# Optimization experiments

Measured on AMD Instinct MI355X. Metric: run time of the kernel, lower is better.

Reference implementation:

```python
import jax, jax.numpy as jnp
import numpy as np

B, S, T, V, E, H = 32, 64, 64, 32000, 512, 1024


def setup_inputs() -> dict:
    key = jax.random.key(0)
    ks = jax.random.split(key, 12)
    n = lambda k, shp, s=0.05: jax.random.normal(k, shp, dtype=jnp.float32) * s
    return {
        "src": jax.random.randint(ks[0], (B, S), 0, V, dtype=jnp.int32),
        "tgt": jax.random.randint(ks[1], (B, T), 0, V, dtype=jnp.int32),
        "enc_emb": n(ks[2], (V, E)),
        "dec_emb": n(ks[3], (V, E)),
        "Wih_e": n(ks[4], (E, H)), "bih_e": jnp.zeros((H,), jnp.float32),
        "Whh_e": n(ks[5], (H, H)), "bhh_e": jnp.zeros((H,), jnp.float32),
        "Wih_d": n(ks[6], (E, H)), "bih_d": jnp.zeros((H,), jnp.float32),
        "Whh_d": n(ks[7], (H, H)), "bhh_d": jnp.zeros((H,), jnp.float32),
        "Wout": n(ks[8], (H, V)), "bout": jnp.zeros((V,), jnp.float32),
    }


def reference(src, tgt, enc_emb, dec_emb, Wih_e, bih_e, Whh_e, bhh_e,
              Wih_d, bih_d, Whh_d, bhh_d, Wout, bout):
    # Embedding lookups: [B, S, E] / [B, T, E]
    src_e = enc_emb[src]
    tgt_e = dec_emb[tgt]
    # Precompute input-to-hidden projections for every timestep (same math,
    # batched into one GEMM each): [B, S, H] / [B, T, H]
    x_e = jnp.einsum('bse,eh->bsh', src_e, Wih_e) + bih_e
    x_d = jnp.einsum('bte,eh->bth', tgt_e, Wih_d) + bih_d

    h0 = jnp.zeros((src.shape[0], Whh_e.shape[0]), dtype=x_e.dtype)

    def enc_step(h, x):  # h,x: [B, H]
        h = jnp.tanh(x + h @ Whh_e + bhh_e)
        return h, None

    h_enc, _ = jax.lax.scan(enc_step, h0, jnp.swapaxes(x_e, 0, 1))

    def dec_step(h, x):
        h = jnp.tanh(x + h @ Whh_d + bhh_d)
        return h, h

    _, hs = jax.lax.scan(dec_step, h_enc, jnp.swapaxes(x_d, 0, 1))  # [T, B, H]

    logits = jnp.einsum('tbh,hv->tbv', hs, Wout) + bout  # [T, B, V]
    out = jax.nn.log_softmax(logits, axis=-1)
    return jnp.swapaxes(out, 0, 1)  # [B, T, V]
```

## Files before the change

kernel.cpp:

```cpp
#include <hip/hip_runtime.h>
#include <hip/hip_bf16.h>
#include <math.h>

#define B_ 32
#define S_ 64
#define T_ 64
#define V_ 32000
#define E_ 512
#define H_ 1024

typedef __attribute__((ext_vector_type(8))) short short8;
typedef __attribute__((ext_vector_type(4))) float f32x4;

static __device__ __forceinline__ unsigned short f2bf(float f) {
  union { float f; unsigned u; } c; c.f = f;
  unsigned r = (c.u + 0x7fffu + ((c.u >> 16) & 1u)) >> 16;
  return (unsigned short)r;
}

__global__ __launch_bounds__(128)
void gather_f32(const int* __restrict__ idx, const float* __restrict__ emb,
                float* __restrict__ dst) {
  int r = blockIdx.x;
  int tid = threadIdx.x;
  int tok = idx[r];
  float4 v = *(const float4*)(emb + (size_t)tok * E_ + tid * 4);
  *(float4*)(dst + (size_t)r * E_ + tid * 4) = v;
}

__global__ __launch_bounds__(256)
void dgemm_bias(const float* __restrict__ A, const float* __restrict__ B,
                const float* __restrict__ bias, float* __restrict__ C,
                int M, int N, int K) {
  __shared__ float As[32][65];
  __shared__ float Bs[32][64];
  const int nbm = M >> 6;
  const int bm = blockIdx.x % nbm;
  const int bn = blockIdx.x / nbm;
  const int tid = threadIdx.x;
  const int tr = tid >> 4, tc = tid & 15;
  double acc[4][4] = {};

  for (int kt = 0; kt < K; kt += 32) {
    {
      int arow = tid >> 3, acol = (tid & 7) * 4;
#pragma unroll
      for (int p = 0; p < 2; ++p) {
        int r = arow + p * 32;
        float4 v = *(const float4*)(A + (size_t)(bm * 64 + r) * K + kt + acol);
        As[acol + 0][r] = v.x; As[acol + 1][r] = v.y;
        As[acol + 2][r] = v.z; As[acol + 3][r] = v.w;
      }
      int brow = tid >> 4, bcol = (tid & 15) * 4;
#pragma unroll
      for (int p = 0; p < 2; ++p) {
        int r = brow + p * 16;
        float4 v = *(const float4*)(B + (size_t)(kt + r) * N + bn * 64 + bcol);
        *(float4*)(&Bs[r][bcol]) = v;
      }
    }
    __syncthreads();
#pragma unroll
    for (int k = 0; k < 32; ++k) {
      double a[4], b[4];
#pragma unroll
      for (int i = 0; i < 4; ++i) a[i] = (double)As[k][tr * 4 + i];
#pragma unroll
      for (int j = 0; j < 4; ++j) b[j] = (double)Bs[k][tc * 4 + j];
#pragma unroll
      for (int i = 0; i < 4; ++i)
#pragma unroll
        for (int j = 0; j < 4; ++j) acc[i][j] = fma(a[i], b[j], acc[i][j]);
    }
    __syncthreads();
  }
#pragma unroll
  for (int i = 0; i < 4; ++i) {
    int gm = bm * 64 + tr * 4 + i;
    int gn = bn * 64 + tc * 4;
    float4 o;
    o.x = (float)(acc[i][0] + (double)bias[gn + 0]);
    o.y = (float)(acc[i][1] + (double)bias[gn + 1]);
    o.z = (float)(acc[i][2] + (double)bias[gn + 2]);
    o.w = (float)(acc[i][3] + (double)bias[gn + 3]);
    *(float4*)(C + (size_t)gm * N + gn) = o;
  }
}

__global__ __launch_bounds__(256)
void transpose_f32(const float* __restrict__ W, float* __restrict__ WT,
                   int K, int N) {
  __shared__ float t[64][65];
  int k0 = blockIdx.x * 64;
  int n0 = blockIdx.y * 64;
  int tid = threadIdx.x;
  int r = tid >> 4, c4 = tid & 15;
#pragma unroll
  for (int i = 0; i < 4; ++i) {
    int row = r + i * 16;
    float4 v = *(const float4*)(W + (size_t)(k0 + row) * N + n0 + c4 * 4);
    t[row][c4 * 4 + 0] = v.x; t[row][c4 * 4 + 1] = v.y;
    t[row][c4 * 4 + 2] = v.z; t[row][c4 * 4 + 3] = v.w;
  }
  __syncthreads();
#pragma unroll
  for (int i = 0; i < 4; ++i) {
    int n = r + i * 16;
    float4 o;
    o.x = t[c4 * 4 + 0][n]; o.y = t[c4 * 4 + 1][n];
    o.z = t[c4 * 4 + 2][n]; o.w = t[c4 * 4 + 3][n];
    *(float4*)(WT + (size_t)(n0 + n) * K + k0 + c4 * 4) = o;
  }
}

__global__ __launch_bounds__(256)
void transpose_bf16(const float* __restrict__ W, unsigned short* __restrict__ WT,
                    int K, int N) {
  __shared__ float t[64][65];
  int k0 = blockIdx.x * 64;
  int n0 = blockIdx.y * 64;
  int tid = threadIdx.x;
  int r = tid >> 4, c4 = tid & 15;
#pragma unroll
  for (int i = 0; i < 4; ++i) {
    int row = r + i * 16;
    float4 v = *(const float4*)(W + (size_t)(k0 + row) * N + n0 + c4 * 4);
    t[row][c4 * 4 + 0] = v.x; t[row][c4 * 4 + 1] = v.y;
    t[row][c4 * 4 + 2] = v.z; t[row][c4 * 4 + 3] = v.w;
  }
  __syncthreads();
#pragma unroll
  for (int i = 0; i < 4; ++i) {
    int n = r + i * 16;
    ushort4 o;
    o.x = f2bf(t[c4 * 4 + 0][n]); o.y = f2bf(t[c4 * 4 + 1][n]);
    o.z = f2bf(t[c4 * 4 + 2][n]); o.w = f2bf(t[c4 * 4 + 3][n]);
    *(ushort4*)(WT + (size_t)(n0 + n) * K + k0 + c4 * 4) = o;
  }
}

__global__ __launch_bounds__(256)
void gemm_bt_swap(const unsigned short* __restrict__ A, const unsigned short* __restrict__ BT,
                  const float* __restrict__ bias, float* __restrict__ C,
                  int M, int N, int K) {
  __shared__ unsigned short As[128 * 64];
  __shared__ unsigned short Bs[128 * 64];
  const int nbm = M >> 7;
  int idx = blockIdx.x;
  const int cpx = gridDim.x >> 3;
  idx = (idx & 7) * cpx + (idx >> 3);
  const int bm = idx % nbm;
  const int bn = idx / nbm;
  const int tid = threadIdx.x;
  const int lane = tid & 63;
  const int wr = (tid >> 6) >> 1;
  const int wc = (tid >> 6) & 1;

  f32x4 acc[4][4] = {};

  for (int kt = 0; kt < K; kt += 64) {
#pragma unroll
    for (int i = 0; i < 4; ++i) {
      int c = i * 256 + tid;
      int row = c >> 3, col8 = c & 7;
      int sw = col8 ^ (row & 7);
      short8 av = *(const short8*)(A + (size_t)(bm * 128 + row) * K + kt + col8 * 8);
      short8 bv = *(const short8*)(BT + (size_t)(bn * 128 + row) * K + kt + col8 * 8);
      *(short8*)(As + row * 64 + sw * 8) = av;
      *(short8*)(Bs + row * 64 + sw * 8) = bv;
    }
    __syncthreads();
#pragma unroll
    for (int kk = 0; kk < 64; kk += 32) {
      int kc = (kk + ((lane >> 4) << 3)) >> 3;
      short8 af[4], bfr[4];
#pragma unroll
      for (int mi = 0; mi < 4; ++mi) {
        int row = wr * 64 + mi * 16 + (lane & 15);
        af[mi] = *(const short8*)(As + row * 64 + ((kc ^ (row & 7)) << 3));
      }
#pragma unroll
      for (int ni = 0; ni < 4; ++ni) {
        int row = wc * 64 + ni * 16 + (lane & 15);
        bfr[ni] = *(const short8*)(Bs + row * 64 + ((kc ^ (row & 7)) << 3));
      }
#pragma unroll
      for (int mi = 0; mi < 4; ++mi)
#pragma unroll
        for (int ni = 0; ni < 4; ++ni)
          acc[mi][ni] = __builtin_amdgcn_mfma_f32_16x16x32_bf16(
              af[mi], bfr[ni], acc[mi][ni], 0, 0, 0);
    }
    __syncthreads();
  }

  const int cq = (lane >> 4) << 2;
  const int cn = lane & 15;
#pragma unroll
  for (int mi = 0; mi < 4; ++mi) {
#pragma unroll
    for (int ni = 0; ni < 4; ++ni) {
      int gn = bn * 128 + wc * 64 + ni * 16 + cn;
      float bv = bias[gn];
#pragma unroll
      for (int q = 0; q < 4; ++q) {
        int gm = bm * 128 + wr * 64 + mi * 16 + cq + q;
        int b = gm & (B_ - 1);
        int t = gm >> 5;
        __builtin_nontemporal_store(acc[mi][ni][q] + bv,
                                    &C[((size_t)b * T_ + t) * N + gn]);
      }
    }
  }
}

__global__ __launch_bounds__(512)
void rnn_scan_grp2(const float* __restrict__ xe, const float* __restrict__ xd,
                   const float* __restrict__ WTe, const float* __restrict__ WTd,
                   const float* __restrict__ bhhE, const float* __restrict__ bhhD,
                   float* __restrict__ hA, float* __restrict__ hB,
                   unsigned short* __restrict__ hsb, unsigned* __restrict__ bar) {
  __shared__ float hl[4 * 1024];
  const int tid = threadIdx.x;
  const int grp = blockIdx.x & 7;
  const int jslot = blockIdx.x >> 3;
  const int jbase = jslot * 32;
  const int bg = grp * 4;
  const int w = tid >> 6;
  const int l = tid & 63;
  unsigned* mybar = bar + grp * 32;

  const int a = 8 * (l & 1) + 4 * ((l >> 1) & 1) + 2 * ((l >> 2) & 1) +
                ((l >> 3) & 1);
  const int lb = a >> 2;
  const int gb = bg + lb;
  const int gj = jbase + w * 4 + (a & 3);
  const float bje = bhhE[gj];
  const float bjd = bhhD[gj];

  float4 wreg[4][4];
  {
    const float* wsrc = WTe + (size_t)(jbase + w * 4) * 1024;
#pragma unroll
    for (int i = 0; i < 4; ++i) {
      int g = l + 64 * i;
#pragma unroll
      for (int ji = 0; ji < 4; ++ji)
        wreg[i][ji] = *(const float4*)(wsrc + (size_t)ji * 1024 + g * 4);
    }
  }

  for (int t = 0; t < 128; ++t) {
    if (t == 64) {
      const float* wsrc = WTd + (size_t)(jbase + w * 4) * 1024;
#pragma unroll
      for (int i = 0; i < 4; ++i) {
        int g = l + 64 * i;
#pragma unroll
        for (int ji = 0; ji < 4; ++ji)
          wreg[i][ji] = *(const float4*)(wsrc + (size_t)ji * 1024 + g * 4);
      }
    }
    const bool enc = (t < 64);
    const int s = t & 63;
    const float* __restrict__ h_in = (t & 1) ? hB : hA;
    float* __restrict__ h_out = (t & 1) ? hA : hB;
    const float* __restrict__ x = enc ? xe : xd;

    float xv = x[((size_t)gb * 64 + s) * H_ + gj];

    {
      const float* hsrc = h_in + bg * H_;
      float v[8];
#pragma unroll
      for (int u = 0; u < 8; ++u)
        v[u] = __hip_atomic_load(hsrc + u * 512 + tid, __ATOMIC_RELAXED,
                                 __HIP_MEMORY_SCOPE_AGENT);
#pragma unroll
      for (int u = 0; u < 8; ++u)
        hl[u * 512 + tid] = v[u];
    }
    __syncthreads();

    double acc[4][4];
#pragma unroll
    for (int bi = 0; bi < 4; ++bi)
#pragma unroll
      for (int ji = 0; ji < 4; ++ji) acc[bi][ji] = 0.;

#pragma unroll
    for (int i = 0; i < 4; ++i) {
      int g = l + 64 * i;
      float4 hv[4];
#pragma unroll
      for (int bi = 0; bi < 4; ++bi)
        hv[bi] = *(const float4*)(hl + bi * 1024 + g * 4);
#pragma unroll
      for (int bi = 0; bi < 4; ++bi)
#pragma unroll
        for (int ji = 0; ji < 4; ++ji) {
          acc[bi][ji] = fma((double)hv[bi].x, (double)wreg[i][ji].x, acc[bi][ji]);
          acc[bi][ji] = fma((double)hv[bi].y, (double)wreg[i][ji].y, acc[bi][ji]);
          acc[bi][ji] = fma((double)hv[bi].z, (double)wreg[i][ji].z, acc[bi][ji]);
          acc[bi][ji] = fma((double)hv[bi].w, (double)wreg[i][ji].w, acc[bi][ji]);
        }
    }

    double r8[8], r4[4], r2[2], r1;
#pragma unroll
    for (int aa = 0; aa < 8; ++aa) {
      double send = (l & 1) ? acc[aa >> 2][aa & 3] : acc[(aa + 8) >> 2][(aa + 8) & 3];
      double mine = (l & 1) ? acc[(aa + 8) >> 2][(aa + 8) & 3] : acc[aa >> 2][aa & 3];
      r8[aa] = mine + __shfl_xor(send, 1);
    }
#pragma unroll
    for (int aa = 0; aa < 4; ++aa) {
      double send = (l & 2) ? r8[aa] : r8[aa + 4];
      double mine = (l & 2) ? r8[aa + 4] : r8[aa];
      r4[aa] = mine + __shfl_xor(send, 2);
    }
#pragma unroll
    for (int aa = 0; aa < 2; ++aa) {
      double send = (l & 4) ? r4[aa] : r4[aa + 2];
      double mine = (l & 4) ? r4[aa + 2] : r4[aa];
      r2[aa] = mine + __shfl_xor(send, 4);
    }
    {
      double send = (l & 8) ? r2[0] : r2[1];
      double mine = (l & 8) ? r2[1] : r2[0];
      r1 = mine + __shfl_xor(send, 8);
    }
    r1 += __shfl_xor(r1, 16);
    r1 += __shfl_xor(r1, 32);

    if (l < 16) {
      double v = r1 + (double)xv + (double)(enc ? bje : bjd);
      double h = tanh(v);
      float hf = (float)h;
      __hip_atomic_store(&h_out[(size_t)gb * H_ + gj], hf, __ATOMIC_RELAXED,
                         __HIP_MEMORY_SCOPE_AGENT);
      if (!enc)
        __builtin_nontemporal_store(f2bf(hf),
                                    &hsb[(size_t)s * (B_ * H_) + gb * H_ + gj]);
    }

    if (t < 127) {
      asm volatile("s_waitcnt vmcnt(0)" ::: "memory");
      __syncthreads();
      if (tid == 0) {
        __hip_atomic_fetch_add(mybar, 1u, __ATOMIC_RELAXED,
                               __HIP_MEMORY_SCOPE_AGENT);
        unsigned tgt = 32u * (unsigned)(t + 1);
        while (__hip_atomic_load(mybar, __ATOMIC_RELAXED,
                                 __HIP_MEMORY_SCOPE_AGENT) < tgt)
          __builtin_amdgcn_s_sleep(1);
      }
      __syncthreads();
    }
  }
}

__global__ __launch_bounds__(512)
void log_softmax_rows(float* __restrict__ out) {
  __shared__ float rl[32000];
  __shared__ float wm[8], wsv[8];
  float* row = out + (size_t)blockIdx.x * V_;
  const int tid = threadIdx.x;
  float m = -INFINITY, s = 0.f;
  for (int i = tid; i < V_ / 4; i += 512) {
    float4 v = *(const float4*)(row + i * 4);
    *(float4*)(rl + i * 4) = v;
    float mx = fmaxf(fmaxf(v.x, v.y), fmaxf(v.z, v.w));
    if (mx > m) { s *= __expf(m - mx); m = mx; }
    s += __expf(v.x - m) + __expf(v.y - m) + __expf(v.z - m) + __expf(v.w - m);
  }
#pragma unroll
  for (int o = 32; o; o >>= 1) {
    float mo = __shfl_xor(m, o);
    float so = __shfl_xor(s, o);
    float mn = fmaxf(m, mo);
    s = s * __expf(m - mn) + so * __expf(mo - mn);
    m = mn;
  }
  int wv = tid >> 6;
  if ((tid & 63) == 0) { wm[wv] = m; wsv[wv] = s; }
  __syncthreads();
  float M = wm[0];
#pragma unroll
  for (int i = 1; i < 8; ++i) M = fmaxf(M, wm[i]);
  float Ssum = 0.f;
#pragma unroll
  for (int i = 0; i < 8; ++i) Ssum += wsv[i] * __expf(wm[i] - M);
  float L = M + logf(Ssum);
  for (int i = tid; i < V_ / 4; i += 512) {
    float4 v = *(const float4*)(rl + i * 4);
    v.x -= L; v.y -= L; v.z -= L; v.w -= L;
    __builtin_nontemporal_store(v.x, &row[i * 4 + 0]);
    __builtin_nontemporal_store(v.y, &row[i * 4 + 1]);
    __builtin_nontemporal_store(v.z, &row[i * 4 + 2]);
    __builtin_nontemporal_store(v.w, &row[i * 4 + 3]);
  }
}

extern "C" void kernel_launch(void* const* d_in, const int* in_sizes, int n_in,
                              void* d_out, int out_size, void* d_ws, size_t ws_size,
                              hipStream_t stream) {
  const int*   src  = (const int*)  d_in[0];
  const int*   tgt  = (const int*)  d_in[1];
  const float* encE = (const float*)d_in[2];
  const float* decE = (const float*)d_in[3];
  const float* WihE = (const float*)d_in[4];
  const float* bihE = (const float*)d_in[5];
  const float* WhhE = (const float*)d_in[6];
  const float* bhhE = (const float*)d_in[7];
  const float* WihD = (const float*)d_in[8];
  const float* bihD = (const float*)d_in[9];
  const float* WhhD = (const float*)d_in[10];
  const float* bhhD = (const float*)d_in[11];
  const float* Wout = (const float*)d_in[12];
  const float* bout = (const float*)d_in[13];
  float* out = (float*)d_out;

  char* w = (char*)d_ws;
  float* x_e = (float*)w;                      w += (size_t)2048 * 1024 * 4;
  float* x_d = (float*)w;                      w += (size_t)2048 * 1024 * 4;
  float* h0  = (float*)w;                      w += 32 * 1024 * 4;
  float* h1  = (float*)w;                      w += 32 * 1024 * 4;
  unsigned* bar = (unsigned*)w;                w += 8 * 32 * 4;
  float* WhhTe = (float*)w;                    w += (size_t)1024 * 1024 * 4;
  float* WhhTd = (float*)w;                    w += (size_t)1024 * 1024 * 4;
  float* AembF = (float*)w;                    w += (size_t)2048 * 512 * 4;
  unsigned short* hsb   = (unsigned short*)w;  w += (size_t)2048 * 1024 * 2;
  unsigned short* WoutT = (unsigned short*)w;  w += (size_t)V_ * 1024 * 2;

  gather_f32<<<B_ * S_, 128, 0, stream>>>(src, encE, AembF);
  dgemm_bias<<<(2048 / 64) * (H_ / 64), 256, 0, stream>>>(AembF, WihE, bihE, x_e,
                                                          2048, H_, E_);
  gather_f32<<<B_ * T_, 128, 0, stream>>>(tgt, decE, AembF);
  dgemm_bias<<<(2048 / 64) * (H_ / 64), 256, 0, stream>>>(AembF, WihD, bihD, x_d,
                                                          2048, H_, E_);

  transpose_f32<<<dim3(H_ / 64, H_ / 64), 256, 0, stream>>>(WhhE, WhhTe, H_, H_);
  transpose_f32<<<dim3(H_ / 64, H_ / 64), 256, 0, stream>>>(WhhD, WhhTd, H_, H_);

  hipMemsetAsync(h0, 0, 32 * 1024 * 4, stream);
  hipMemsetAsync(bar, 0, 8 * 32 * 4, stream);
  rnn_scan_grp2<<<256, 512, 0, stream>>>(x_e, x_d, WhhTe, WhhTd, bhhE, bhhD,
                                         h0, h1, hsb, bar);

  transpose_bf16<<<dim3(H_ / 64, V_ / 64), 256, 0, stream>>>(Wout, WoutT, H_, V_);
  gemm_bt_swap<<<(2048 / 128) * (V_ / 128), 256, 0, stream>>>(hsb, WoutT, bout, out,
                                                              2048, V_, H_);
  log_softmax_rows<<<B_ * T_, 512, 0, stream>>>(out);
}
```

Measured before the change: 1.128 ms.

## Pipeline RNN scan per batch row with per-row barriers and prefetch

The RNN scan kernel now processes one batch row at a time, cycling through four rows per group with a separate barrier counter for each row. Each row's hidden-state and x loads for the next phase are prefetched while the current row's dot products run. Arrival signalling is deferred so other blocks' work on one row can overlap this block's work on another. The point is to hide global barrier latency behind compute across independent batch rows. In exchange there are four times as many barrier phases, each doing less compute, and the synchronisation ordering is more delicate.

```diff
diff --git a/kernel.cpp b/kernel.cpp
--- a/kernel.cpp
+++ b/kernel.cpp
@@ -215,7 +215,7 @@
 }
 
 __global__ __launch_bounds__(512)
-void rnn_scan_grp2(const float* __restrict__ xe, const float* __restrict__ xd,
+void rnn_scan_pipe(const float* __restrict__ xe, const float* __restrict__ xd,
                    const float* __restrict__ WTe, const float* __restrict__ WTd,
                    const float* __restrict__ bhhE, const float* __restrict__ bhhD,
                    float* __restrict__ hA, float* __restrict__ hB,
@@ -225,16 +225,11 @@
   const int grp = blockIdx.x & 7;
   const int jslot = blockIdx.x >> 3;
   const int jbase = jslot * 32;
-  const int bg = grp * 4;
   const int w = tid >> 6;
   const int l = tid & 63;
-  unsigned* mybar = bar + grp * 32;
-
-  const int a = 8 * (l & 1) + 4 * ((l >> 1) & 1) + 2 * ((l >> 2) & 1) +
-                ((l >> 3) & 1);
-  const int lb = a >> 2;
-  const int gb = bg + lb;
-  const int gj = jbase + w * 4 + (a & 3);
+
+  const int ji_own = 2 * (l & 1) + ((l >> 1) & 1);
+  const int gj = jbase + w * 4 + ji_own;
   const float bje = bhhE[gj];
   const float bjd = bhhD[gj];
 
@@ -250,8 +245,21 @@
     }
   }
 
-  for (int t = 0; t < 128; ++t) {
-    if (t == 64) {
+  float v0, v1, xv = 0.f;
+  {
+    const float* hsrc = hA + (size_t)(grp * 4) * H_;
+    v0 = __hip_atomic_load(hsrc + tid, __ATOMIC_RELAXED, __HIP_MEMORY_SCOPE_AGENT);
+    v1 = __hip_atomic_load(hsrc + 512 + tid, __ATOMIC_RELAXED, __HIP_MEMORY_SCOPE_AGENT);
+    if (l < 4) xv = xe[((size_t)(grp * 4) * 64 + 0) * H_ + gj];
+  }
+
+  for (int p = 0; p < 512; ++p) {
+    const int t = p >> 2, c = p & 3;
+    const bool enc = (t < 64);
+    const int s = t & 63;
+    const int cg = grp * 4 + c;
+
+    if (p == 256) {
       const float* wsrc = WTd + (size_t)(jbase + w * 4) * 1024;
 #pragma unroll
       for (int i = 0; i < 4; ++i) {
@@ -261,101 +269,82 @@
           wreg[i][ji] = *(const float4*)(wsrc + (size_t)ji * 1024 + g * 4);
       }
     }
-    const bool enc = (t < 64);
-    const int s = t & 63;
-    const float* __restrict__ h_in = (t & 1) ? hB : hA;
-    float* __restrict__ h_out = (t & 1) ? hA : hB;
-    const float* __restrict__ x = enc ? xe : xd;
-
-    float xv = x[((size_t)gb * 64 + s) * H_ + gj];
-
-    {
-      const float* hsrc = h_in + bg * H_;
-      float v[8];
-#pragma unroll
-      for (int u = 0; u < 8; ++u)
-        v[u] = __hip_atomic_load(hsrc + u * 512 + tid, __ATOMIC_RELAXED,
-                                 __HIP_MEMORY_SCOPE_AGENT);
-#pragma unroll
-      for (int u = 0; u < 8; ++u)
-        hl[u * 512 + tid] = v[u];
-    }
-    __syncthreads();
-
-    double acc[4][4];
-#pragma unroll
-    for (int bi = 0; bi < 4; ++bi)
-#pragma unroll
-      for (int ji = 0; ji < 4; ++ji) acc[bi][ji] = 0.;
-
+
+    hl[c * 1024 + tid] = v0;
+    hl[c * 1024 + 512 + tid] = v1;
+    const float xcur = xv;
+
+    const int p1 = p + 1;
+    const int t1 = p1 >> 2, c1 = p1 & 3;
+    if (p1 < 512 && tid == 0) {
+      unsigned tgt = 32u * (unsigned)t1;
+      unsigned* g = bar + (size_t)(grp * 4 + c1) * 32;
+      while (__hip_atomic_load(g, __ATOMIC_RELAXED, __HIP_MEMORY_SCOPE_AGENT) < tgt)
+        __builtin_amdgcn_s_sleep(1);
+    }
+    asm volatile("s_waitcnt lgkmcnt(0)" ::: "memory");
+    __builtin_amdgcn_s_barrier();
+    __builtin_amdgcn_sched_barrier(0);
+
+    if (p1 < 512) {
+      const int cg1 = grp * 4 + c1;
+      const float* hin1 = ((t1 & 1) ? hB : hA) + (size_t)cg1 * H_;
+      v0 = __hip_atomic_load(hin1 + tid, __ATOMIC_RELAXED, __HIP_MEMORY_SCOPE_AGENT);
+      v1 = __hip_atomic_load(hin1 + 512 + tid, __ATOMIC_RELAXED, __HIP_MEMORY_SCOPE_AGENT);
+      if (l < 4) {
+        const float* x1 = (t1 < 64) ? xe : xd;
+        xv = x1[((size_t)cg1 * 64 + (t1 & 63)) * H_ + gj];
+      }
+    }
+
+    double acc[4] = {0., 0., 0., 0.};
 #pragma unroll
     for (int i = 0; i < 4; ++i) {
       int g = l + 64 * i;
-      float4 hv[4];
-#pragma unroll
-      for (int bi = 0; bi < 4; ++bi)
-        hv[bi] = *(const float4*)(hl + bi * 1024 + g * 4);
-#pragma unroll
-      for (int bi = 0; bi < 4; ++bi)
-#pragma unroll
-        for (int ji = 0; ji < 4; ++ji) {
-          acc[bi][ji] = fma((double)hv[bi].x, (double)wreg[i][ji].x, acc[bi][ji]);
-          acc[bi][ji] = fma((double)hv[bi].y, (double)wreg[i][ji].y, acc[bi][ji]);
-          acc[bi][ji] = fma((double)hv[bi].z, (double)wreg[i][ji].z, acc[bi][ji]);
-          acc[bi][ji] = fma((double)hv[bi].w, (double)wreg[i][ji].w, acc[bi][ji]);
-        }
-    }
-
-    double r8[8], r4[4], r2[2], r1;
-#pragma unroll
-    for (int aa = 0; aa < 8; ++aa) {
-      double send = (l & 1) ? acc[aa >> 2][aa & 3] : acc[(aa + 8) >> 2][(aa + 8) & 3];
-      double mine = (l & 1) ? acc[(aa + 8) >> 2][(aa + 8) & 3] : acc[aa >> 2][aa & 3];
-      r8[aa] = mine + __shfl_xor(send, 1);
-    }
-#pragma unroll
-    for (int aa = 0; aa < 4; ++aa) {
-      double send = (l & 2) ? r8[aa] : r8[aa + 4];
-      double mine = (l & 2) ? r8[aa + 4] : r8[aa];
-      r4[aa] = mine + __shfl_xor(send, 2);
-    }
+      float4 hv = *(const float4*)(hl + c * 1024 + g * 4);
+#pragma unroll
+      for (int ji = 0; ji < 4; ++ji) {
+        acc[ji] = fma((double)hv.x, (double)wreg[i][ji].x, acc[ji]);
+        acc[ji] = fma((double)hv.y, (double)wreg[i][ji].y, acc[ji]);
+        acc[ji] = fma((double)hv.z, (double)wreg[i][ji].z, acc[ji]);
+        acc[ji] = fma((double)hv.w, (double)wreg[i][ji].w, acc[ji]);
+      }
+    }
+
+    double r2[2], r1;
 #pragma unroll
     for (int aa = 0; aa < 2; ++aa) {
-      double send = (l & 4) ? r4[aa] : r4[aa + 2];
-      double mine = (l & 4) ? r4[aa + 2] : r4[aa];
-      r2[aa] = mine + __shfl_xor(send, 4);
+      double send = (l & 1) ? acc[aa] : acc[aa + 2];
+      double mine = (l & 1) ? acc[aa + 2] : acc[aa];
+      r2[aa] = mine + __shfl_xor(send, 1);
     }
     {
-      double send = (l & 8) ? r2[0] : r2[1];
-      double mine = (l & 8) ? r2[1] : r2[0];
-      r1 = mine + __shfl_xor(send, 8);
-    }
+      double send = (l & 2) ? r2[0] : r2[1];
+      double mine = (l & 2) ? r2[1] : r2[0];
+      r1 = mine + __shfl_xor(send, 2);
+    }
+    r1 += __shfl_xor(r1, 4);
+    r1 += __shfl_xor(r1, 8);
     r1 += __shfl_xor(r1, 16);
     r1 += __shfl_xor(r1, 32);
 
-    if (l < 16) {
-      double v = r1 + (double)xv + (double)(enc ? bje : bjd);
-      double h = tanh(v);
+    asm volatile("s_waitcnt vmcnt(3)" ::: "memory");
+    __builtin_amdgcn_s_barrier();
+    __builtin_amdgcn_sched_barrier(0);
+    if (p > 0 && tid == 0)
+      __hip_atomic_fetch_add(bar + (size_t)(grp * 4 + ((p - 1) & 3)) * 32, 1u,
+                             __ATOMIC_RELAXED, __HIP_MEMORY_SCOPE_AGENT);
+
+    if (l < 4) {
+      double vv = r1 + (double)xcur + (double)(enc ? bje : bjd);
+      double h = tanh(vv);
       float hf = (float)h;
-      __hip_atomic_store(&h_out[(size_t)gb * H_ + gj], hf, __ATOMIC_RELAXED,
+      float* hout = (t & 1) ? hA : hB;
+      __hip_atomic_store(&hout[(size_t)cg * H_ + gj], hf, __ATOMIC_RELAXED,
                          __HIP_MEMORY_SCOPE_AGENT);
       if (!enc)
         __builtin_nontemporal_store(f2bf(hf),
-                                    &hsb[(size_t)s * (B_ * H_) + gb * H_ + gj]);
-    }
-
-    if (t < 127) {
-      asm volatile("s_waitcnt vmcnt(0)" ::: "memory");
-      __syncthreads();
-      if (tid == 0) {
-        __hip_atomic_fetch_add(mybar, 1u, __ATOMIC_RELAXED,
-                               __HIP_MEMORY_SCOPE_AGENT);
-        unsigned tgt = 32u * (unsigned)(t + 1);
-        while (__hip_atomic_load(mybar, __ATOMIC_RELAXED,
-                                 __HIP_MEMORY_SCOPE_AGENT) < tgt)
-          __builtin_amdgcn_s_sleep(1);
-      }
-      __syncthreads();
+                                    &hsb[(size_t)s * (B_ * H_) + (size_t)cg * H_ + gj]);
     }
   }
 }
@@ -426,7 +415,7 @@
   float* x_d = (float*)w;                      w += (size_t)2048 * 1024 * 4;
   float* h0  = (float*)w;                      w += 32 * 1024 * 4;
   float* h1  = (float*)w;                      w += 32 * 1024 * 4;
-  unsigned* bar = (unsigned*)w;                w += 8 * 32 * 4;
+  unsigned* bar = (unsigned*)w;                w += 32 * 32 * 4;
   float* WhhTe = (float*)w;                    w += (size_t)1024 * 1024 * 4;
   float* WhhTd = (float*)w;                    w += (size_t)1024 * 1024 * 4;
   float* AembF = (float*)w;                    w += (size_t)2048 * 512 * 4;
@@ -444,8 +433,8 @@
   transpose_f32<<<dim3(H_ / 64, H_ / 64), 256, 0, stream>>>(WhhD, WhhTd, H_, H_);
 
   hipMemsetAsync(h0, 0, 32 * 1024 * 4, stream);
-  hipMemsetAsync(bar, 0, 8 * 32 * 4, stream);
-  rnn_scan_grp2<<<256, 512, 0, stream>>>(x_e, x_d, WhhTe, WhhTd, bhhE, bhhD,
+  hipMemsetAsync(bar, 0, 32 * 32 * 4, stream);
+  rnn_scan_pipe<<<256, 512, 0, stream>>>(x_e, x_d, WhhTe, WhhTd, bhhE, bhhD,
                                          h0, h1, hsb, bar);
 
   transpose_bf16<<<dim3(H_ / 64, V_ / 64), 256, 0, stream>>>(Wout, WoutT, H_, V_);
```

Result: slower. 1.603 ms (+42.1%).

## Split RNN scan across 512 blocks with 16 hidden units each

Applied to the files above, without the earlier changes.

The recurrent scan kernel now launches 512 blocks instead of 256. Each block owns 16 hidden columns instead of 32, so each thread holds half the weight registers and does half the FP64 FMAs per step. The shuffle reduction tree is reshaped to match, the per-group barrier target doubles to 64, and the bf16 hs store is moved after the barrier so it stays off the critical path. The dgemm shared-memory A tile is padded to 68 columns so it can be read as float4 vectors. In exchange, more blocks take part in every grid barrier, which raises sync overhead, and all 512 blocks must be co-resident for the spin barrier to avoid deadlock.

```diff
diff --git a/kernel.cpp b/kernel.cpp
--- a/kernel.cpp
+++ b/kernel.cpp
@@ -32,7 +32,7 @@
 void dgemm_bias(const float* __restrict__ A, const float* __restrict__ B,
                 const float* __restrict__ bias, float* __restrict__ C,
                 int M, int N, int K) {
-  __shared__ float As[32][65];
+  __shared__ float As[32][68];
   __shared__ float Bs[32][64];
   const int nbm = M >> 6;
   const int bm = blockIdx.x % nbm;
@@ -62,11 +62,10 @@
     __syncthreads();
 #pragma unroll
     for (int k = 0; k < 32; ++k) {
-      double a[4], b[4];
-#pragma unroll
-      for (int i = 0; i < 4; ++i) a[i] = (double)As[k][tr * 4 + i];
-#pragma unroll
-      for (int j = 0; j < 4; ++j) b[j] = (double)Bs[k][tc * 4 + j];
+      float4 av = *(const float4*)(&As[k][tr * 4]);
+      float4 bv = *(const float4*)(&Bs[k][tc * 4]);
+      double a[4] = {(double)av.x, (double)av.y, (double)av.z, (double)av.w};
+      double b[4] = {(double)bv.x, (double)bv.y, (double)bv.z, (double)bv.w};
 #pragma unroll
       for (int i = 0; i < 4; ++i)
 #pragma unroll
@@ -214,50 +213,50 @@
   }
 }
 
-__global__ __launch_bounds__(512)
-void rnn_scan_grp2(const float* __restrict__ xe, const float* __restrict__ xd,
-                   const float* __restrict__ WTe, const float* __restrict__ WTd,
-                   const float* __restrict__ bhhE, const float* __restrict__ bhhD,
-                   float* __restrict__ hA, float* __restrict__ hB,
-                   unsigned short* __restrict__ hsb, unsigned* __restrict__ bar) {
+__global__ __launch_bounds__(512, 4)
+void rnn_scan_split(const float* __restrict__ xe, const float* __restrict__ xd,
+                    const float* __restrict__ WTe, const float* __restrict__ WTd,
+                    const float* __restrict__ bhhE, const float* __restrict__ bhhD,
+                    float* __restrict__ hA, float* __restrict__ hB,
+                    unsigned short* __restrict__ hsb, unsigned* __restrict__ bar) {
   __shared__ float hl[4 * 1024];
   const int tid = threadIdx.x;
-  const int grp = blockIdx.x & 7;
-  const int jslot = blockIdx.x >> 3;
-  const int jbase = jslot * 32;
+  const int half = blockIdx.x >> 8;
+  const int grp = (blockIdx.x & 7) ^ half;
+  const int jslot = ((blockIdx.x >> 3) & 31) + (half << 5);
+  const int jbase = jslot * 16;
   const int bg = grp * 4;
   const int w = tid >> 6;
   const int l = tid & 63;
   unsigned* mybar = bar + grp * 32;
 
-  const int a = 8 * (l & 1) + 4 * ((l >> 1) & 1) + 2 * ((l >> 2) & 1) +
-                ((l >> 3) & 1);
-  const int lb = a >> 2;
+  const int a = 4 * (l & 1) + 2 * ((l >> 1) & 1) + ((l >> 2) & 1);
+  const int lb = a >> 1;
   const int gb = bg + lb;
-  const int gj = jbase + w * 4 + (a & 3);
+  const int gj = jbase + w * 2 + (a & 1);
   const float bje = bhhE[gj];
   const float bjd = bhhD[gj];
 
-  float4 wreg[4][4];
+  float4 wreg[4][2];
   {
-    const float* wsrc = WTe + (size_t)(jbase + w * 4) * 1024;
+    const float* wsrc = WTe + (size_t)(jbase + w * 2) * 1024;
 #pragma unroll
     for (int i = 0; i < 4; ++i) {
       int g = l + 64 * i;
 #pragma unroll
-      for (int ji = 0; ji < 4; ++ji)
+      for (int ji = 0; ji < 2; ++ji)
         wreg[i][ji] = *(const float4*)(wsrc + (size_t)ji * 1024 + g * 4);
     }
   }
 
   for (int t = 0; t < 128; ++t) {
     if (t == 64) {
-      const float* wsrc = WTd + (size_t)(jbase + w * 4) * 1024;
+      const float* wsrc = WTd + (size_t)(jbase + w * 2) * 1024;
 #pragma unroll
       for (int i = 0; i < 4; ++i) {
         int g = l + 64 * i;
 #pragma unroll
-        for (int ji = 0; ji < 4; ++ji)
+        for (int ji = 0; ji < 2; ++ji)
           wreg[i][ji] = *(const float4*)(wsrc + (size_t)ji * 1024 + g * 4);
       }
     }
@@ -282,11 +281,11 @@
     }
     __syncthreads();
 
-    double acc[4][4];
+    double acc[4][2];
 #pragma unroll
     for (int bi = 0; bi < 4; ++bi)
 #pragma unroll
-      for (int ji = 0; ji < 4; ++ji) acc[bi][ji] = 0.;
+      for (int ji = 0; ji < 2; ++ji) acc[bi][ji] = 0.;
 
 #pragma unroll
     for (int i = 0; i < 4; ++i) {
@@ -298,7 +297,7 @@
 #pragma unroll
       for (int bi = 0; bi < 4; ++bi)
 #pragma unroll
-        for (int ji = 0; ji < 4; ++ji) {
+        for (int ji = 0; ji < 2; ++ji) {
           acc[bi][ji] = fma((double)hv[bi].x, (double)wreg[i][ji].x, acc[bi][ji]);
           acc[bi][ji] = fma((double)hv[bi].y, (double)wreg[i][ji].y, acc[bi][ji]);
           acc[bi][ji] = fma((double)hv[bi].z, (double)wreg[i][ji].z, acc[bi][ji]);
@@ -306,42 +305,37 @@
         }
     }
 
-    double r8[8], r4[4], r2[2], r1;
-#pragma unroll
-    for (int aa = 0; aa < 8; ++aa) {
-      double send = (l & 1) ? acc[aa >> 2][aa & 3] : acc[(aa + 8) >> 2][(aa + 8) & 3];
-      double mine = (l & 1) ? acc[(aa + 8) >> 2][(aa + 8) & 3] : acc[aa >> 2][aa & 3];
-      r8[aa] = mine + __shfl_xor(send, 1);
-    }
+    double r4_[4], r2_[2], r1;
 #pragma unroll
     for (int aa = 0; aa < 4; ++aa) {
-      double send = (l & 2) ? r8[aa] : r8[aa + 4];
-      double mine = (l & 2) ? r8[aa + 4] : r8[aa];
-      r4[aa] = mine + __shfl_xor(send, 2);
+      double lo = acc[aa >> 1][aa & 1];
+      double hi = acc[(aa + 4) >> 1][(aa + 4) & 1];
+      double send = (l & 1) ? lo : hi;
+      double mine = (l & 1) ? hi : lo;
+      r4_[aa] = mine + __shfl_xor(send, 1);
     }
 #pragma unroll
     for (int aa = 0; aa < 2; ++aa) {
-      double send = (l & 4) ? r4[aa] : r4[aa + 2];
-      double mine = (l & 4) ? r4[aa + 2] : r4[aa];
-      r2[aa] = mine + __shfl_xor(send, 4);
+      double send = (l & 2) ? r4_[aa] : r4_[aa + 2];
+      double mine = (l & 2) ? r4_[aa + 2] : r4_[aa];
+      r2_[aa] = mine + __shfl_xor(send, 2);
     }
     {
-      double send = (l & 8) ? r2[0] : r2[1];
-      double mine = (l & 8) ? r2[1] : r2[0];
-      r1 = mine + __shfl_xor(send, 8);
-    }
+      double send = (l & 4) ? r2_[0] : r2_[1];
+      double mine = (l & 4) ? r2_[1] : r2_[0];
+      r1 = mine + __shfl_xor(send, 4);
+    }
+    r1 += __shfl_xor(r1, 8);
     r1 += __shfl_xor(r1, 16);
     r1 += __shfl_xor(r1, 32);
 
-    if (l < 16) {
-      double v = r1 + (double)xv + (double)(enc ? bje : bjd);
-      double h = tanh(v);
-      float hf = (float)h;
+    float hf = 0.f;
+    if (l < 8) {
+      double vv = r1 + (double)xv + (double)(enc ? bje : bjd);
+      double h = tanh(vv);
+      hf = (float)h;
       __hip_atomic_store(&h_out[(size_t)gb * H_ + gj], hf, __ATOMIC_RELAXED,
                          __HIP_MEMORY_SCOPE_AGENT);
-      if (!enc)
-        __builtin_nontemporal_store(f2bf(hf),
-                                    &hsb[(size_t)s * (B_ * H_) + gb * H_ + gj]);
     }
 
     if (t < 127) {
@@ -350,13 +344,16 @@
       if (tid == 0) {
         __hip_atomic_fetch_add(mybar, 1u, __ATOMIC_RELAXED,
                                __HIP_MEMORY_SCOPE_AGENT);
-        unsigned tgt = 32u * (unsigned)(t + 1);
+        unsigned tgt = 64u * (unsigned)(t + 1);
         while (__hip_atomic_load(mybar, __ATOMIC_RELAXED,
                                  __HIP_MEMORY_SCOPE_AGENT) < tgt)
           __builtin_amdgcn_s_sleep(1);
       }
       __syncthreads();
     }
+    if (!enc && l < 8)
+      __builtin_nontemporal_store(f2bf(hf),
+                                  &hsb[(size_t)s * (B_ * H_) + (size_t)gb * H_ + gj]);
   }
 }
 
@@ -445,8 +442,8 @@
 
   hipMemsetAsync(h0, 0, 32 * 1024 * 4, stream);
   hipMemsetAsync(bar, 0, 8 * 32 * 4, stream);
-  rnn_scan_grp2<<<256, 512, 0, stream>>>(x_e, x_d, WhhTe, WhhTd, bhhE, bhhD,
-                                         h0, h1, hsb, bar);
+  rnn_scan_split<<<512, 512, 0, stream>>>(x_e, x_d, WhhTe, WhhTd, bhhE, bhhD,
+                                          h0, h1, hsb, bar);
 
   transpose_bf16<<<dim3(H_ / 64, V_ / 64), 256, 0, stream>>>(Wout, WoutT, H_, V_);
   gemm_bt_swap<<<(2048 / 128) * (V_ / 128), 256, 0, stream>>>(hsb, WoutT, bout, out,
```

Measured after the change: 1.687 ms. 49.5% more time.
